# Kernel optimization log

Hardware: AMD Instinct MI355X
Metric: run time of the kernel (lower is better)

## Reference

```python
import jax, jax.numpy as jnp
import numpy as np

N_NODES = 100_000
N_RAND_EDGES = 1_600_000
NEG_SLOPE = 0.2


def setup_inputs() -> dict:
    key = jax.random.key(0)
    ks = jax.random.split(key, 12)
    inputs = jax.random.normal(ks[0], (N_NODES, 128), dtype=jnp.float32)
    # params (fc weight [in, H*D], attn vectors [H, D]); 0.1 scale for stability
    W0 = jax.random.normal(ks[1], (128, 4 * 32), dtype=jnp.float32) * 0.1
    al0 = jax.random.normal(ks[2], (4, 32), dtype=jnp.float32) * 0.1
    ar0 = jax.random.normal(ks[3], (4, 32), dtype=jnp.float32) * 0.1
    W1 = jax.random.normal(ks[4], (4 * 32, 4 * 32), dtype=jnp.float32) * 0.1
    al1 = jax.random.normal(ks[5], (4, 32), dtype=jnp.float32) * 0.1
    ar1 = jax.random.normal(ks[6], (4, 32), dtype=jnp.float32) * 0.1
    W2 = jax.random.normal(ks[7], (4 * 32, 1 * 40), dtype=jnp.float32) * 0.1
    al2 = jax.random.normal(ks[8], (1, 40), dtype=jnp.float32) * 0.1
    ar2 = jax.random.normal(ks[9], (1, 40), dtype=jnp.float32) * 0.1
    # edge list: random edges + self loops (guarantees in-degree >= 1)
    src = jnp.concatenate([
        jax.random.randint(ks[10], (N_RAND_EDGES,), 0, N_NODES, dtype=jnp.int32),
        jnp.arange(N_NODES, dtype=jnp.int32)])
    dst = jnp.concatenate([
        jax.random.randint(ks[11], (N_RAND_EDGES,), 0, N_NODES, dtype=jnp.int32),
        jnp.arange(N_NODES, dtype=jnp.int32)])
    return dict(inputs=inputs, W0=W0, al0=al0, ar0=ar0, W1=W1, al1=al1,
                ar1=ar1, W2=W2, al2=al2, ar2=ar2, src=src, dst=dst, empty=0)


def _gat_conv(h, W, al, ar, src, dst):
    """DGL-style GATConv (no dropout, no residual, no bias). Returns [N, H, D]."""
    N = h.shape[0]
    H, D = al.shape
    feat = (h @ W).reshape(N, H, D)
    el = jnp.sum(feat * al, axis=-1)  # [N, H]
    er = jnp.sum(feat * ar, axis=-1)  # [N, H]
    e = jax.nn.leaky_relu(el[src] + er[dst], negative_slope=NEG_SLOPE)  # [E, H]
    # edge softmax over incoming edges of each destination node (stable)
    m = jax.ops.segment_max(e, dst, num_segments=N)          # [N, H]
    ee = jnp.exp(e - m[dst])                                 # [E, H]
    denom = jax.ops.segment_sum(ee, dst, num_segments=N)     # [N, H]
    alpha = ee / denom[dst]                                  # [E, H]
    # gather source features, weight by attention, scatter-sum to destinations
    out = jax.ops.segment_sum(feat[src] * alpha[:, :, None], dst, num_segments=N)
    return out


def reference(inputs, W0, al0, ar0, W1, al1, ar1, W2, al2, ar2, src, dst, empty):
    N = inputs.shape[0]
    h = inputs
    for (W, al, ar) in ((W0, al0, ar0), (W1, al1, ar1)):
        h = jax.nn.elu(_gat_conv(h, W, al, ar, src, dst)).reshape(N, -1)
    logits = _gat_conv(h, W2, al2, ar2, src, dst).mean(axis=1)  # [N, num_classes]
    return jax.nn.log_softmax(logits, axis=1)
```

## Files before the change

### kernel.cpp

```cpp
#include <hip/hip_runtime.h>
#include <math.h>

typedef unsigned int uint32;
typedef unsigned short ushort;

__device__ inline uint32 bf16rn(float x){
  uint32 b = __float_as_uint(x);
  return (b + 0x7fffu + ((b>>16)&1u)) >> 16;
}
__device__ inline float bf16lo(uint32 v){ return __uint_as_float(v<<16); }
__device__ inline float bf16hi(uint32 v){ return __uint_as_float(v & 0xffff0000u); }

#define BKT_SHIFT 9
#define BKTCAP 12288
#define PCHUNK 8192

__global__ __launch_bounds__(256) void k_partition(const int* __restrict__ src, const int* __restrict__ dst,
                        int* __restrict__ bkt_cursor, uint32* __restrict__ pairs, int E){
  __shared__ int cnt[512];
  __shared__ int base[512];
  int t = threadIdx.x;
  int blockBase = blockIdx.x * PCHUNK;
  for (int i=t; i<512; i+=256) cnt[i]=0;
  __syncthreads();
  #pragma unroll
  for (int i=0; i<PCHUNK/1024; i++){
    int e0 = blockBase + (i*256 + t)*4;
    if (e0+3 < E){
      int4 d4 = *(const int4*)&dst[e0];
      atomicAdd(&cnt[d4.x>>BKT_SHIFT],1);
      atomicAdd(&cnt[d4.y>>BKT_SHIFT],1);
      atomicAdd(&cnt[d4.z>>BKT_SHIFT],1);
      atomicAdd(&cnt[d4.w>>BKT_SHIFT],1);
    } else {
      for (int e=e0; e<E && e<e0+4; e++) atomicAdd(&cnt[dst[e]>>BKT_SHIFT],1);
    }
  }
  __syncthreads();
  for (int i=t; i<512; i+=256){
    int c = cnt[i];
    base[i] = c ? atomicAdd(&bkt_cursor[i], c) : 0;
    cnt[i] = 0;
  }
  __syncthreads();
  #pragma unroll
  for (int i=0; i<PCHUNK/1024; i++){
    int e0 = blockBase + (i*256 + t)*4;
    if (e0+3 < E){
      int4 s4 = *(const int4*)&src[e0];
      int4 d4 = *(const int4*)&dst[e0];
      int bx, pos;
      bx=d4.x>>BKT_SHIFT; pos=base[bx]+atomicAdd(&cnt[bx],1); if(pos<BKTCAP) pairs[(size_t)bx*BKTCAP+pos]=(uint32)s4.x|((uint32)(d4.x&511)<<22);
      bx=d4.y>>BKT_SHIFT; pos=base[bx]+atomicAdd(&cnt[bx],1); if(pos<BKTCAP) pairs[(size_t)bx*BKTCAP+pos]=(uint32)s4.y|((uint32)(d4.y&511)<<22);
      bx=d4.z>>BKT_SHIFT; pos=base[bx]+atomicAdd(&cnt[bx],1); if(pos<BKTCAP) pairs[(size_t)bx*BKTCAP+pos]=(uint32)s4.z|((uint32)(d4.z&511)<<22);
      bx=d4.w>>BKT_SHIFT; pos=base[bx]+atomicAdd(&cnt[bx],1); if(pos<BKTCAP) pairs[(size_t)bx*BKTCAP+pos]=(uint32)s4.w|((uint32)(d4.w&511)<<22);
    } else {
      for (int e=e0; e<E && e<e0+4; e++){
        int s=src[e], d=dst[e];
        int bx=d>>BKT_SHIFT; int pos=base[bx]+atomicAdd(&cnt[bx],1);
        if(pos<BKTCAP) pairs[(size_t)bx*BKTCAP+pos]=(uint32)s|((uint32)(d&511)<<22);
      }
    }
  }
}

__global__ __launch_bounds__(512) void k_scanbkt(const int* __restrict__ bkt_cursor, int nb,
                      int* __restrict__ bucket_base, int* __restrict__ row_ptr, int N){
  __shared__ int sc[512];
  int t = threadIdx.x;
  int v = (t<nb) ? min(bkt_cursor[t], BKTCAP) : 0;
  sc[t]=v; __syncthreads();
  int x=v;
  for (int off=1; off<512; off<<=1){
    int y=(t>=off)? sc[t-off]:0;
    __syncthreads();
    x+=y; sc[t]=x;
    __syncthreads();
  }
  if (t<nb) bucket_base[t] = x - v;
  if (t==511) row_ptr[N] = x;
}

__global__ __launch_bounds__(1024) void k_build(const int* __restrict__ bkt_cursor,
                        const int* __restrict__ bucket_base, const uint32* __restrict__ pairs,
                        int* __restrict__ row_ptr, int* __restrict__ csr_src, int N){
  __shared__ int hist[512];
  __shared__ int sc[512];
  __shared__ int cur[512];
  int b = blockIdx.x;
  int t = threadIdx.x;
  int cnt = bkt_cursor[b]; if (cnt > BKTCAP) cnt = BKTCAP;
  int base = bucket_base[b];
  const uint32* p = pairs + (size_t)b*BKTCAP;
  if (t<512) hist[t]=0;
  __syncthreads();
  for (int i=t; i<cnt; i+=1024) atomicAdd(&hist[p[i]>>22], 1);
  __syncthreads();
  int v = (t<512)? hist[t] : 0;
  if (t<512) sc[t]=v;
  __syncthreads();
  int x=v;
  for (int off=1; off<512; off<<=1){
    int y = (t<512 && t>=off)? sc[t-off] : 0;
    __syncthreads();
    if (t<512){ x+=y; sc[t]=x; }
    __syncthreads();
  }
  if (t<512){
    int excl = x - v;
    int gnode = (b<<BKT_SHIFT) + t;
    if (gnode < N) row_ptr[gnode] = base + excl;
    cur[t] = excl;
  }
  __syncthreads();
  for (int i=t; i<cnt; i+=1024){
    uint32 e = p[i];
    int pos = atomicAdd(&cur[e>>22], 1);
    csr_src[base + pos] = (int)(e & 0x3FFFFFu);
  }
}

template<bool BF16A>
__global__ __launch_bounds__(256) void k_gemm128T(const void* __restrict__ Av, const float* __restrict__ W,
                                                 const float* __restrict__ al, const float* __restrict__ ar,
                                                 ushort* __restrict__ Fb,
                                                 float* __restrict__ el, float* __restrict__ er, int N){
  __shared__ float hs[32][68];
  __shared__ float ws[32][128];
  int t = threadIdx.x;
  int rowBase = blockIdx.x*64;
  int rg8 = (t>>5)*8;
  int cq  = (t&31)*4;
  float acc[8][4] = {};
  for (int kc=0; kc<128; kc+=32){
    {
      int row = t>>2; int kk = (t&3)*8;
      int grow = rowBase+row;
      float a8[8];
      if (grow < N){
        if constexpr (BF16A){
          const ushort* Ab = (const ushort*)Av;
          uint4 u = *(const uint4*)&Ab[(size_t)grow*128 + kc + kk];
          a8[0]=bf16lo(u.x); a8[1]=bf16hi(u.x); a8[2]=bf16lo(u.y); a8[3]=bf16hi(u.y);
          a8[4]=bf16lo(u.z); a8[5]=bf16hi(u.z); a8[6]=bf16lo(u.w); a8[7]=bf16hi(u.w);
        } else {
          const float* Af = (const float*)Av;
          float4 v0 = *(const float4*)&Af[(size_t)grow*128 + kc + kk];
          float4 v1 = *(const float4*)&Af[(size_t)grow*128 + kc + kk + 4];
          a8[0]=v0.x; a8[1]=v0.y; a8[2]=v0.z; a8[3]=v0.w;
          a8[4]=v1.x; a8[5]=v1.y; a8[6]=v1.z; a8[7]=v1.w;
        }
      } else {
        #pragma unroll
        for (int j=0;j<8;j++) a8[j]=0.f;
      }
      #pragma unroll
      for (int j=0;j<8;j++) hs[kk+j][row]=a8[j];
    }
    {
      int k = t>>3; int c0 = (t&7)*16;
      const float4* wp = (const float4*)&W[(size_t)(kc+k)*128 + c0];
      float4 w0=wp[0], w1=wp[1], w2=wp[2], w3=wp[3];
      *(float4*)&ws[k][c0+ 0]=w0; *(float4*)&ws[k][c0+ 4]=w1;
      *(float4*)&ws[k][c0+ 8]=w2; *(float4*)&ws[k][c0+12]=w3;
    }
    __syncthreads();
    #pragma unroll
    for (int k=0;k<32;k++){
      float4 bv  = *(const float4*)&ws[k][cq];
      float4 av0 = *(const float4*)&hs[k][rg8];
      float4 av1 = *(const float4*)&hs[k][rg8+4];
      float a8[8] = {av0.x,av0.y,av0.z,av0.w,av1.x,av1.y,av1.z,av1.w};
      float b4[4] = {bv.x,bv.y,bv.z,bv.w};
      #pragma unroll
      for (int r=0;r<8;r++)
        #pragma unroll
        for (int c=0;c<4;c++)
          acc[r][c] = fmaf(a8[r], b4[c], acc[r][c]);
    }
    __syncthreads();
  }
  float al4[4], ar4[4];
  #pragma unroll
  for (int i=0;i<4;i++){ al4[i]=al[cq+i]; ar4[i]=ar[cq+i]; }
  int c = t&31;
  int h = c>>3;
  int rowTop = rowBase + rg8;
  #pragma unroll
  for (int r=0;r<8;r++){
    int row = rowTop + r;
    if (row < N){
      uint32 u0 = bf16rn(acc[r][0]) | (bf16rn(acc[r][1])<<16);
      uint32 u1 = bf16rn(acc[r][2]) | (bf16rn(acc[r][3])<<16);
      *(uint2*)(Fb + (size_t)row*128 + cq) = make_uint2(u0,u1);
    }
    float pl = acc[r][0]*al4[0]+acc[r][1]*al4[1]+acc[r][2]*al4[2]+acc[r][3]*al4[3];
    float pr = acc[r][0]*ar4[0]+acc[r][1]*ar4[1]+acc[r][2]*ar4[2]+acc[r][3]*ar4[3];
    pl += __shfl_xor(pl,1); pr += __shfl_xor(pr,1);
    pl += __shfl_xor(pl,2); pr += __shfl_xor(pr,2);
    pl += __shfl_xor(pl,4); pr += __shfl_xor(pr,4);
    if ((c&7)==0 && row < N){ el[(size_t)row*4+h]=pl; er[(size_t)row*4+h]=pr; }
  }
}

__global__ __launch_bounds__(256) void k_agg128(const uint32* __restrict__ Fu, const float* __restrict__ el,
                         const float* __restrict__ er, const int* __restrict__ row_ptr,
                         const int* __restrict__ csr_src, ushort* __restrict__ out, int N){
  __shared__ float wlds[4][272];
  int t = threadIdx.x;
  int lane = t & 63;
  int wv = t >> 6;
  int node = (blockIdx.x*blockDim.x + t)>>6;
  if (__builtin_amdgcn_readfirstlane(node) >= N) return;
  int h = lane>>4;
  int i0 = lane & 15;
  float erv = er[(size_t)node*4+h];
  int beg = row_ptr[node], end = row_ptr[node+1];
  int ubeg = __builtin_amdgcn_readfirstlane(beg);
  int uend = __builtin_amdgcn_readfirstlane(end);
  int udeg = uend - ubeg;
  int sv = (lane < udeg) ? csr_src[ubeg+lane] : 0;
  int sn[4]; float evv[4];
  #pragma unroll
  for (int j=0;j<4;j++) sn[j] = __shfl(sv, i0 + 16*j);
  #pragma unroll
  for (int j=0;j<4;j++) evv[j] = el[(size_t)sn[j]*4+h];
  float w4[4];
  #pragma unroll
  for (int j=0;j<4;j++){
    float ev = evv[j] + erv;
    ev = ev>0.f ? ev : 0.2f*ev;
    w4[j] = (i0 + 16*j < udeg) ? __expf(ev) : 0.f;
  }
  float dsum = (w4[0]+w4[1]) + (w4[2]+w4[3]);
  dsum += __shfl_xor(dsum, 1);
  dsum += __shfl_xor(dsum, 2);
  dsum += __shfl_xor(dsum, 4);
  dsum += __shfl_xor(dsum, 8);
  int wb = h*68 + i0;
  wlds[wv][wb   ] = w4[0];
  wlds[wv][wb+16] = w4[1];
  wlds[wv][wb+32] = w4[2];
  wlds[wv][wb+48] = w4[3];
  const int* sp = csr_src + ubeg;
  const float* wp = &wlds[wv][h*68];
  float acc0=0.f, acc1=0.f;
  int nm = udeg > 64 ? 64 : udeg;
  uint32 vb[8];
  #pragma unroll
  for (int k=0;k<8;k++) vb[k] = (k<nm) ? Fu[(size_t)sp[k]*64 + lane] : 0u;
  int i=0;
  for (; i+16<=nm; i+=8){
    uint32 vn[8];
    #pragma unroll
    for (int k=0;k<8;k++) vn[k] = Fu[(size_t)sp[i+8+k]*64 + lane];
    #pragma unroll
    for (int k=0;k<8;k++){
      float wi = wp[i+k];
      acc0 = fmaf(wi, bf16lo(vb[k]), acc0);
      acc1 = fmaf(wi, bf16hi(vb[k]), acc1);
    }
    #pragma unroll
    for (int k=0;k<8;k++) vb[k]=vn[k];
  }
  {
    int lim = nm - i; if (lim > 8) lim = 8;
    #pragma unroll
    for (int k=0;k<8;k++) if (k<lim){
      float wi = wp[i+k];
      acc0 = fmaf(wi, bf16lo(vb[k]), acc0);
      acc1 = fmaf(wi, bf16hi(vb[k]), acc1);
    }
    for (int e=i+8; e<nm; e++){
      float wi = wp[e];
      uint32 v = Fu[(size_t)sp[e]*64 + lane];
      acc0 = fmaf(wi, bf16lo(v), acc0);
      acc1 = fmaf(wi, bf16hi(v), acc1);
    }
  }
  if (udeg > 64){
    for (int e=64; e<udeg; e++){
      int s = sp[e];
      float x = el[(size_t)s*4+h] + erv;
      x = x>0.f?x:0.2f*x; x=__expf(x);
      uint32 v = Fu[(size_t)s*64+lane];
      dsum += x;
      acc0 = fmaf(x, bf16lo(v), acc0);
      acc1 = fmaf(x, bf16hi(v), acc1);
    }
  }
  float inv = 1.0f/dsum;
  float o0 = acc0*inv, o1 = acc1*inv;
  o0 = o0>0.f ? o0 : expm1f(o0);
  o1 = o1>0.f ? o1 : expm1f(o1);
  uint32 uo = bf16rn(o0) | (bf16rn(o1)<<16);
  *(uint32*)(out + (size_t)node*128 + lane*2) = uo;
}

__global__ __launch_bounds__(256) void k_gemm42(const ushort* __restrict__ A, const float* __restrict__ W,
                        const float* __restrict__ al, const float* __restrict__ ar,
                        ushort* __restrict__ Fb, float* __restrict__ el, float* __restrict__ er, int N){
  __shared__ float wfull[128*48];
  __shared__ float hs[32][132];
  int t = threadIdx.x;
  int rowBase = blockIdx.x*128;
  for (int i=t; i<1280; i+=256){
    float4 v = *(const float4*)&W[i*4];
    int g = i*4;
    *(float4*)&wfull[(g/40)*48 + (g%40)] = v;
  }
  {
    int k = t & 127;
    const float* wrow = W + k*40;
    const float* a = (t < 128) ? al : ar;
    float s = 0.f;
    #pragma unroll
    for (int c=0;c<40;c++) s += wrow[c]*a[c];
    if (t < 128){
      wfull[k*48+40] = s;
      wfull[k*48+42] = 0.f; wfull[k*48+43] = 0.f; wfull[k*48+44] = 0.f;
    } else {
      wfull[k*48+41] = s;
      wfull[k*48+45] = 0.f; wfull[k*48+46] = 0.f; wfull[k*48+47] = 0.f;
    }
  }
  int c0 = (t&7)*6;
  int r0 = (t>>3)*4;
  float acc[4][6] = {};
  for (int kc=0; kc<128; kc+=32){
    {
      int row = t>>1; int kk0 = (t&1)*16;
      int grow = rowBase + row;
      if (grow < N){
        uint4 u0 = *(const uint4*)&A[(size_t)grow*128 + kc + kk0];
        uint4 u1 = *(const uint4*)&A[(size_t)grow*128 + kc + kk0 + 8];
        hs[kk0+ 0][row]=bf16lo(u0.x); hs[kk0+ 1][row]=bf16hi(u0.x);
        hs[kk0+ 2][row]=bf16lo(u0.y); hs[kk0+ 3][row]=bf16hi(u0.y);
        hs[kk0+ 4][row]=bf16lo(u0.z); hs[kk0+ 5][row]=bf16hi(u0.z);
        hs[kk0+ 6][row]=bf16lo(u0.w); hs[kk0+ 7][row]=bf16hi(u0.w);
        hs[kk0+ 8][row]=bf16lo(u1.x); hs[kk0+ 9][row]=bf16hi(u1.x);
        hs[kk0+10][row]=bf16lo(u1.y); hs[kk0+11][row]=bf16hi(u1.y);
        hs[kk0+12][row]=bf16lo(u1.z); hs[kk0+13][row]=bf16hi(u1.z);
        hs[kk0+14][row]=bf16lo(u1.w); hs[kk0+15][row]=bf16hi(u1.w);
      } else {
        #pragma unroll
        for (int j=0;j<16;j++) hs[kk0+j][row]=0.f;
      }
    }
    __syncthreads();
    #pragma unroll
    for (int k=0;k<32;k++){
      float4 av = *(const float4*)&hs[k][r0];
      const float* wp = &wfull[(kc+k)*48 + c0];
      float2 b01 = *(const float2*)&wp[0];
      float2 b23 = *(const float2*)&wp[2];
      float2 b45 = *(const float2*)&wp[4];
      float a4[4] = {av.x,av.y,av.z,av.w};
      float b6[6] = {b01.x,b01.y,b23.x,b23.y,b45.x,b45.y};
      #pragma unroll
      for (int r=0;r<4;r++)
        #pragma unroll
        for (int c=0;c<6;c++)
          acc[r][c] = fmaf(a4[r], b6[c], acc[r][c]);
    }
    __syncthreads();
  }
  #pragma unroll
  for (int r=0;r<4;r++){
    int row = rowBase + r0 + r;
    if (row >= N) break;
    if (c0 < 40){
      #pragma unroll
      for (int j=0;j<6;j+=2){
        int col = c0 + j;
        if (col < 40){
          uint32 u = bf16rn(acc[r][j]) | (bf16rn(acc[r][j+1])<<16);
          *(uint32*)(Fb + (size_t)row*40 + col) = u;
        }
      }
      if (c0 == 36){ el[row] = acc[r][4]; er[row] = acc[r][5]; }
    }
  }
}

__global__ __launch_bounds__(256) void k_agg40(const ushort* __restrict__ Fb, const float* __restrict__ el,
                       const float* __restrict__ er, const int* __restrict__ row_ptr,
                       const int* __restrict__ csr_src, float* __restrict__ out, int N){
  __shared__ float wlds[4][64];
  int t = threadIdx.x;
  int lane = t & 63;
  int wv = t >> 6;
  int node = (blockIdx.x*blockDim.x + t)>>6;
  if (__builtin_amdgcn_readfirstlane(node) >= N) return;
  bool act = lane<40;
  int l40 = act ? lane : 0;
  float erv = er[node];
  int beg = row_ptr[node], end = row_ptr[node+1];
  int ubeg = __builtin_amdgcn_readfirstlane(beg);
  int uend = __builtin_amdgcn_readfirstlane(end);
  int udeg = uend - ubeg;
  int sv = (lane < udeg) ? csr_src[ubeg+lane] : 0;
  float w = 0.f;
  if (lane < udeg){
    float ev = el[sv] + erv;
    ev = ev>0.f ? ev : 0.2f*ev;
    w = __expf(ev);
  }
  float dsum = w;
  dsum += __shfl_xor(dsum, 1);
  dsum += __shfl_xor(dsum, 2);
  dsum += __shfl_xor(dsum, 4);
  dsum += __shfl_xor(dsum, 8);
  dsum += __shfl_xor(dsum, 16);
  dsum += __shfl_xor(dsum, 32);
  wlds[wv][lane] = w;
  const int* sp = csr_src + ubeg;
  float acc=0.f;
  int nm = udeg > 64 ? 64 : udeg;
  ushort fb8[8];
  #pragma unroll
  for (int k=0;k<8;k++) fb8[k] = (k<nm) ? Fb[(size_t)sp[k]*40 + l40] : (ushort)0;
  int i=0;
  for (; i+16<=nm; i+=8){
    ushort fn[8];
    #pragma unroll
    for (int k=0;k<8;k++) fn[k] = Fb[(size_t)sp[i+8+k]*40 + l40];
    #pragma unroll
    for (int k=0;k<8;k++){
      float wi = wlds[wv][i+k];
      acc = fmaf(wi, __uint_as_float(((uint32)fb8[k])<<16), acc);
    }
    #pragma unroll
    for (int k=0;k<8;k++) fb8[k]=fn[k];
  }
  {
    int lim = nm - i; if (lim > 8) lim = 8;
    #pragma unroll
    for (int k=0;k<8;k++) if (k<lim){
      float wi = wlds[wv][i+k];
      acc = fmaf(wi, __uint_as_float(((uint32)fb8[k])<<16), acc);
    }
    for (int e=i+8; e<nm; e++){
      float wi = wlds[wv][e];
      ushort f = Fb[(size_t)sp[e]*40 + l40];
      acc = fmaf(wi, __uint_as_float(((uint32)f)<<16), acc);
    }
  }
  if (udeg > 64){
    for (int e=64; e<udeg; e++){
      int s = sp[e];
      float x = el[s] + erv;
      x = x>0.f?x:0.2f*x; x=__expf(x);
      ushort f = Fb[(size_t)s*40 + l40];
      dsum += x;
      acc = fmaf(x, __uint_as_float(((uint32)f)<<16), acc);
    }
  }
  float logit = acc/dsum;
  float m = act ? logit : -INFINITY;
  for (int off=32; off; off>>=1) m = fmaxf(m, __shfl_xor(m, off));
  float ex = act ? expf(logit - m) : 0.f;
  float ssum = ex;
  for (int off=32; off; off>>=1) ssum += __shfl_xor(ssum, off);
  if (act) out[(size_t)node*40 + lane] = logit - m - logf(ssum);
}

extern "C" void kernel_launch(void* const* d_in, const int* in_sizes, int n_in,
                              void* d_out, int out_size, void* d_ws, size_t ws_size,
                              hipStream_t stream){
  const float* inputs = (const float*)d_in[0];
  const float* W0  = (const float*)d_in[1];
  const float* al0 = (const float*)d_in[2];
  const float* ar0 = (const float*)d_in[3];
  const float* W1  = (const float*)d_in[4];
  const float* al1 = (const float*)d_in[5];
  const float* ar1 = (const float*)d_in[6];
  const float* W2  = (const float*)d_in[7];
  const float* al2 = (const float*)d_in[8];
  const float* ar2 = (const float*)d_in[9];
  const int* src = (const int*)d_in[10];
  const int* dst = (const int*)d_in[11];
  int N = in_sizes[0]/128;
  int E = in_sizes[10];
  int NB = (N + (1<<BKT_SHIFT) - 1) >> BKT_SHIFT;

  char* p = (char*)d_ws;
  auto carve = [&](size_t bytes)->char*{ char* q=p; p += ((bytes+255)/256)*256; return q; };
  ushort* Fb   = (ushort*)carve((size_t)N*128*2);
  ushort* Fb40 = (ushort*)carve((size_t)N*40*2);
  ushort* bufH = (ushort*)carve((size_t)N*128*2);
  float* el  = (float*)carve((size_t)N*4*4);
  float* er  = (float*)carve((size_t)N*4*4);
  float* el2 = (float*)carve((size_t)N*4);
  float* er2 = (float*)carve((size_t)N*4);
  int* bkt_cursor  = (int*)carve((size_t)NB*4);
  int* bucket_base = (int*)carve((size_t)NB*4);
  int* row_ptr = (int*)carve((size_t)(N+1)*4);
  int* csr_src = (int*)carve((size_t)E*4);

  uint32* pairs = (uint32*)bufH;

  hipMemsetAsync(bkt_cursor, 0, (size_t)NB*4, stream);
  int nPB = (E + PCHUNK - 1) / PCHUNK;
  k_partition<<<nPB, 256, 0, stream>>>(src, dst, bkt_cursor, pairs, E);
  k_scanbkt  <<<1, 512, 0, stream>>>(bkt_cursor, NB, bucket_base, row_ptr, N);
  k_build    <<<NB, 1024, 0, stream>>>(bkt_cursor, bucket_base, pairs, row_ptr, csr_src, N);

  int gRows = (N+63)/64;
  int gWave = (N+3)/4;
  int gRows42 = (N+127)/128;
  k_gemm128T<false><<<gRows,256,0,stream>>>(inputs, W0, al0, ar0, Fb, el, er, N);
  k_agg128 <<<gWave,256,0,stream>>>((const uint32*)Fb, el, er, row_ptr, csr_src, bufH, N);
  k_gemm128T<true><<<gRows,256,0,stream>>>(bufH, W1, al1, ar1, Fb, el, er, N);
  k_agg128 <<<gWave,256,0,stream>>>((const uint32*)Fb, el, er, row_ptr, csr_src, bufH, N);
  k_gemm42 <<<gRows42,256,0,stream>>>(bufH, W2, al2, ar2, Fb40, el2, er2, N);
  k_agg40  <<<gWave,256,0,stream>>>(Fb40, el2, er2, row_ptr, csr_src, (float*)d_out, N);
}
```

Baseline: 406.9 us.

## Replace FP32 FMA GEMM with bf16 MFMA kernel and pad layer-3 feature stride

The two 128x128 projection GEMMs now convert the weights and activations to bf16, store them in XOR-swizzled LDS, and compute with 16x16x32 bf16 MFMA instructions instead of scalar FP32 FMAs. The attention logits el/er are reduced from the MFMA accumulators with cross-lane shuffles and written as float4. Separately, the 40-wide layer-3 feature buffer is padded to a 64-element row stride, which aligns its rows for the gathers in the final aggregation. The costs are a per-block weight conversion into 32KB of LDS, which may limit occupancy, and lower precision because the layer-0 inputs are now rounded to bf16.

```diff
diff --git a/kernel.cpp b/kernel.cpp
--- a/kernel.cpp
+++ b/kernel.cpp
@@ -3,6 +3,8 @@
 
 typedef unsigned int uint32;
 typedef unsigned short ushort;
+typedef __attribute__((ext_vector_type(8))) short short8;
+typedef __attribute__((ext_vector_type(4))) float f32x4;
 
 __device__ inline uint32 bf16rn(float x){
   uint32 b = __float_as_uint(x);
@@ -14,6 +16,7 @@
 #define BKT_SHIFT 9
 #define BKTCAP 12288
 #define PCHUNK 8192
+#define FB40S 64
 
 __global__ __launch_bounds__(256) void k_partition(const int* __restrict__ src, const int* __restrict__ dst,
                         int* __restrict__ bkt_cursor, uint32* __restrict__ pairs, int E){
@@ -121,85 +124,103 @@
 }
 
 template<bool BF16A>
-__global__ __launch_bounds__(256) void k_gemm128T(const void* __restrict__ Av, const float* __restrict__ W,
-                                                 const float* __restrict__ al, const float* __restrict__ ar,
-                                                 ushort* __restrict__ Fb,
-                                                 float* __restrict__ el, float* __restrict__ er, int N){
-  __shared__ float hs[32][68];
-  __shared__ float ws[32][128];
+__global__ __launch_bounds__(256) void k_gemm128_mfma(const void* __restrict__ Av, const float* __restrict__ W,
+                        const float* __restrict__ al, const float* __restrict__ ar,
+                        ushort* __restrict__ Fb, float* __restrict__ el, float* __restrict__ er, int N){
+  __shared__ __align__(16) ushort Wlds[128*128];
+  __shared__ __align__(16) ushort Alds[64*128];
+  __shared__ float sal[128], sar[128];
   int t = threadIdx.x;
   int rowBase = blockIdx.x*64;
-  int rg8 = (t>>5)*8;
-  int cq  = (t&31)*4;
-  float acc[8][4] = {};
-  for (int kc=0; kc<128; kc+=32){
-    {
-      int row = t>>2; int kk = (t&3)*8;
-      int grow = rowBase+row;
-      float a8[8];
-      if (grow < N){
-        if constexpr (BF16A){
-          const ushort* Ab = (const ushort*)Av;
-          uint4 u = *(const uint4*)&Ab[(size_t)grow*128 + kc + kk];
-          a8[0]=bf16lo(u.x); a8[1]=bf16hi(u.x); a8[2]=bf16lo(u.y); a8[3]=bf16hi(u.y);
-          a8[4]=bf16lo(u.z); a8[5]=bf16hi(u.z); a8[6]=bf16lo(u.w); a8[7]=bf16hi(u.w);
-        } else {
-          const float* Af = (const float*)Av;
-          float4 v0 = *(const float4*)&Af[(size_t)grow*128 + kc + kk];
-          float4 v1 = *(const float4*)&Af[(size_t)grow*128 + kc + kk + 4];
-          a8[0]=v0.x; a8[1]=v0.y; a8[2]=v0.z; a8[3]=v0.w;
-          a8[4]=v1.x; a8[5]=v1.y; a8[6]=v1.z; a8[7]=v1.w;
+  for (int i=t; i<8192; i+=256){
+    int col = i & 127;
+    int k2  = (i >> 7) * 2;
+    float w0 = W[(size_t)k2*128 + col];
+    float w1 = W[(size_t)(k2+1)*128 + col];
+    uint32 pk = bf16rn(w0) | (bf16rn(w1)<<16);
+    int byte = col*256 + k2*2;
+    byte ^= (col&7)<<4;
+    *(uint32*)((char*)Wlds + byte) = pk;
+  }
+  if (t < 128){ sal[t] = al[t]; sar[t] = ar[t]; }
+  {
+    int row = t>>2, k0 = (t&3)*32;
+    int grow = rowBase + row;
+    uint32 pk[16];
+    if (grow < N){
+      if constexpr (BF16A){
+        const ushort* Ab = (const ushort*)Av;
+        const uint4* ap = (const uint4*)(Ab + (size_t)grow*128 + k0);
+        #pragma unroll
+        for (int q=0;q<4;q++){ uint4 u = ap[q]; pk[q*4]=u.x; pk[q*4+1]=u.y; pk[q*4+2]=u.z; pk[q*4+3]=u.w; }
+      } else {
+        const float* Af = (const float*)Av;
+        #pragma unroll
+        for (int j=0;j<16;j++){
+          float2 v = *(const float2*)(Af + (size_t)grow*128 + k0 + j*2);
+          pk[j] = bf16rn(v.x) | (bf16rn(v.y)<<16);
         }
-      } else {
-        #pragma unroll
-        for (int j=0;j<8;j++) a8[j]=0.f;
       }
+    } else {
       #pragma unroll
-      for (int j=0;j<8;j++) hs[kk+j][row]=a8[j];
-    }
-    {
-      int k = t>>3; int c0 = (t&7)*16;
-      const float4* wp = (const float4*)&W[(size_t)(kc+k)*128 + c0];
-      float4 w0=wp[0], w1=wp[1], w2=wp[2], w3=wp[3];
-      *(float4*)&ws[k][c0+ 0]=w0; *(float4*)&ws[k][c0+ 4]=w1;
-      *(float4*)&ws[k][c0+ 8]=w2; *(float4*)&ws[k][c0+12]=w3;
-    }
-    __syncthreads();
-    #pragma unroll
-    for (int k=0;k<32;k++){
-      float4 bv  = *(const float4*)&ws[k][cq];
-      float4 av0 = *(const float4*)&hs[k][rg8];
-      float4 av1 = *(const float4*)&hs[k][rg8+4];
-      float a8[8] = {av0.x,av0.y,av0.z,av0.w,av1.x,av1.y,av1.z,av1.w};
-      float b4[4] = {bv.x,bv.y,bv.z,bv.w};
-      #pragma unroll
-      for (int r=0;r<8;r++)
-        #pragma unroll
-        for (int c=0;c<4;c++)
-          acc[r][c] = fmaf(a8[r], b4[c], acc[r][c]);
-    }
-    __syncthreads();
-  }
-  float al4[4], ar4[4];
-  #pragma unroll
-  for (int i=0;i<4;i++){ al4[i]=al[cq+i]; ar4[i]=ar[cq+i]; }
-  int c = t&31;
-  int h = c>>3;
-  int rowTop = rowBase + rg8;
-  #pragma unroll
-  for (int r=0;r<8;r++){
-    int row = rowTop + r;
+      for (int j=0;j<16;j++) pk[j]=0u;
+    }
+    #pragma unroll
+    for (int q=0;q<4;q++){
+      int byte = row*256 + (k0 + q*8)*2;
+      byte ^= (row&7)<<4;
+      *(uint4*)((char*)Alds + byte) = make_uint4(pk[q*4],pk[q*4+1],pk[q*4+2],pk[q*4+3]);
+    }
+  }
+  __syncthreads();
+  int wid = t>>6, lane = t&63;
+  int strip = wid*16;
+  int lrow = lane & 15;
+  int lk   = (lane>>4)*8;
+  int swz  = (lrow&7)<<4;
+  f32x4 acc[8];
+  #pragma unroll
+  for (int tc=0; tc<8; tc++) acc[tc] = (f32x4){0.f,0.f,0.f,0.f};
+  #pragma unroll
+  for (int kstep=0; kstep<4; kstep++){
+    int kb = (kstep*32 + lk)*2;
+    short8 bfrag = *(const short8*)((const char*)Alds + (((strip+lrow)*256 + kb) ^ swz));
+    #pragma unroll
+    for (int tc=0; tc<8; tc++){
+      short8 afrag = *(const short8*)((const char*)Wlds + (((tc*16+lrow)*256 + kb) ^ swz));
+      acc[tc] = __builtin_amdgcn_mfma_f32_16x16x32_bf16(afrag, bfrag, acc[tc], 0, 0, 0);
+    }
+  }
+  int row = rowBase + strip + lrow;
+  int cq = (lane>>4)*4;
+  #pragma unroll
+  for (int tc=0; tc<8; tc++){
     if (row < N){
-      uint32 u0 = bf16rn(acc[r][0]) | (bf16rn(acc[r][1])<<16);
-      uint32 u1 = bf16rn(acc[r][2]) | (bf16rn(acc[r][3])<<16);
-      *(uint2*)(Fb + (size_t)row*128 + cq) = make_uint2(u0,u1);
-    }
-    float pl = acc[r][0]*al4[0]+acc[r][1]*al4[1]+acc[r][2]*al4[2]+acc[r][3]*al4[3];
-    float pr = acc[r][0]*ar4[0]+acc[r][1]*ar4[1]+acc[r][2]*ar4[2]+acc[r][3]*ar4[3];
-    pl += __shfl_xor(pl,1); pr += __shfl_xor(pr,1);
-    pl += __shfl_xor(pl,2); pr += __shfl_xor(pr,2);
-    pl += __shfl_xor(pl,4); pr += __shfl_xor(pr,4);
-    if ((c&7)==0 && row < N){ el[(size_t)row*4+h]=pl; er[(size_t)row*4+h]=pr; }
+      uint32 u0 = bf16rn(acc[tc][0]) | (bf16rn(acc[tc][1])<<16);
+      uint32 u1 = bf16rn(acc[tc][2]) | (bf16rn(acc[tc][3])<<16);
+      *(uint2*)(Fb + (size_t)row*128 + tc*16 + cq) = make_uint2(u0,u1);
+    }
+  }
+  float hl[4] = {0.f,0.f,0.f,0.f};
+  float hr[4] = {0.f,0.f,0.f,0.f};
+  #pragma unroll
+  for (int tc=0; tc<8; tc++){
+    int cbase = tc*16 + cq;
+    int h = tc>>1;
+    #pragma unroll
+    for (int r=0;r<4;r++){
+      hl[h] = fmaf(acc[tc][r], sal[cbase+r], hl[h]);
+      hr[h] = fmaf(acc[tc][r], sar[cbase+r], hr[h]);
+    }
+  }
+  #pragma unroll
+  for (int h=0;h<4;h++){
+    hl[h] += __shfl_xor(hl[h],16); hl[h] += __shfl_xor(hl[h],32);
+    hr[h] += __shfl_xor(hr[h],16); hr[h] += __shfl_xor(hr[h],32);
+  }
+  if (lane < 16 && row < N){
+    *(float4*)&el[(size_t)row*4] = make_float4(hl[0],hl[1],hl[2],hl[3]);
+    *(float4*)&er[(size_t)row*4] = make_float4(hr[0],hr[1],hr[2],hr[3]);
   }
 }
 
@@ -375,7 +396,7 @@
         int col = c0 + j;
         if (col < 40){
           uint32 u = bf16rn(acc[r][j]) | (bf16rn(acc[r][j+1])<<16);
-          *(uint32*)(Fb + (size_t)row*40 + col) = u;
+          *(uint32*)(Fb + (size_t)row*FB40S + col) = u;
         }
       }
       if (c0 == 36){ el[row] = acc[r][4]; er[row] = acc[r][5]; }
@@ -419,12 +440,12 @@
   int nm = udeg > 64 ? 64 : udeg;
   ushort fb8[8];
   #pragma unroll
-  for (int k=0;k<8;k++) fb8[k] = (k<nm) ? Fb[(size_t)sp[k]*40 + l40] : (ushort)0;
+  for (int k=0;k<8;k++) fb8[k] = (k<nm) ? Fb[(size_t)sp[k]*FB40S + l40] : (ushort)0;
   int i=0;
   for (; i+16<=nm; i+=8){
     ushort fn[8];
     #pragma unroll
-    for (int k=0;k<8;k++) fn[k] = Fb[(size_t)sp[i+8+k]*40 + l40];
+    for (int k=0;k<8;k++) fn[k] = Fb[(size_t)sp[i+8+k]*FB40S + l40];
     #pragma unroll
     for (int k=0;k<8;k++){
       float wi = wlds[wv][i+k];
@@ -442,7 +463,7 @@
     }
     for (int e=i+8; e<nm; e++){
       float wi = wlds[wv][e];
-      ushort f = Fb[(size_t)sp[e]*40 + l40];
+      ushort f = Fb[(size_t)sp[e]*FB40S + l40];
       acc = fmaf(wi, __uint_as_float(((uint32)f)<<16), acc);
     }
   }
@@ -451,7 +472,7 @@
       int s = sp[e];
       float x = el[s] + erv;
       x = x>0.f?x:0.2f*x; x=__expf(x);
-      ushort f = Fb[(size_t)s*40 + l40];
+      ushort f = Fb[(size_t)s*FB40S + l40];
       dsum += x;
       acc = fmaf(x, __uint_as_float(((uint32)f)<<16), acc);
     }
@@ -487,7 +508,7 @@
   char* p = (char*)d_ws;
   auto carve = [&](size_t bytes)->char*{ char* q=p; p += ((bytes+255)/256)*256; return q; };
   ushort* Fb   = (ushort*)carve((size_t)N*128*2);
-  ushort* Fb40 = (ushort*)carve((size_t)N*40*2);
+  ushort* Fb40 = (ushort*)carve((size_t)N*FB40S*2);
   ushort* bufH = (ushort*)carve((size_t)N*128*2);
   float* el  = (float*)carve((size_t)N*4*4);
   float* er  = (float*)carve((size_t)N*4*4);
@@ -509,9 +530,9 @@
   int gRows = (N+63)/64;
   int gWave = (N+3)/4;
   int gRows42 = (N+127)/128;
-  k_gemm128T<false><<<gRows,256,0,stream>>>(inputs, W0, al0, ar0, Fb, el, er, N);
+  k_gemm128_mfma<false><<<gRows,256,0,stream>>>(inputs, W0, al0, ar0, Fb, el, er, N);
   k_agg128 <<<gWave,256,0,stream>>>((const uint32*)Fb, el, er, row_ptr, csr_src, bufH, N);
-  k_gemm128T<true><<<gRows,256,0,stream>>>(bufH, W1, al1, ar1, Fb, el, er, N);
+  k_gemm128_mfma<true><<<gRows,256,0,stream>>>(bufH, W1, al1, ar1, Fb, el, er, N);
   k_agg128 <<<gWave,256,0,stream>>>((const uint32*)Fb, el, er, row_ptr, csr_src, bufH, N);
   k_gemm42 <<<gRows42,256,0,stream>>>(bufH, W2, al2, ar2, Fb40, el2, er2, N);
   k_agg40  <<<gWave,256,0,stream>>>(Fb40, el2, er2, row_ptr, csr_src, (float*)d_out, N);
```

Result: faster. 350.8 us (-13.8%).
